# Kernel tuning notes

Hardware: AMD Instinct MI355X
Metric: run time of the kernel (lower is better)

## Reference

```python
import jax, jax.numpy as jnp
import numpy as np

B, N, D = 16, 1024, 768
NEG = -1.0e9

def leaky_relu(x, slope=0.01):
    return jnp.where(x >= 0, x, slope * x)

def setup_inputs() -> dict:
    key = jax.random.key(0)
    ks = jax.random.split(key, 20)
    s = 0.02
    inp = {
        'inputs': jax.random.normal(ks[0], (B, N, D), dtype=jnp.float32),
        'adj_mat': jax.random.randint(ks[1], (B, N, N), 0, 2).astype(jnp.float32),
        # BaseGraphAttNet params
        'W_fc': jax.random.normal(ks[2], (D, D), dtype=jnp.float32) * s,
        'b_fc': jnp.zeros((D,), dtype=jnp.float32),
        'w_q': jax.random.normal(ks[3], (D,), dtype=jnp.float32) * s,
        'b_q': jnp.zeros((), dtype=jnp.float32),
        'w_k': jax.random.normal(ks[4], (D,), dtype=jnp.float32) * s,
        'b_k': jnp.zeros((), dtype=jnp.float32),
        # gating params (6 linears)
        'W_uy': jax.random.normal(ks[5], (D, D), dtype=jnp.float32) * s,
        'b_uy': jnp.zeros((D,), dtype=jnp.float32),
        'W_ux': jax.random.normal(ks[6], (D, D), dtype=jnp.float32) * s,
        'b_ux': jnp.zeros((D,), dtype=jnp.float32),
        'W_ry': jax.random.normal(ks[7], (D, D), dtype=jnp.float32) * s,
        'b_ry': jnp.zeros((D,), dtype=jnp.float32),
        'W_rx': jax.random.normal(ks[8], (D, D), dtype=jnp.float32) * s,
        'b_rx': jnp.zeros((D,), dtype=jnp.float32),
        'W_ty': jax.random.normal(ks[9], (D, D), dtype=jnp.float32) * s,
        'b_ty': jnp.zeros((D,), dtype=jnp.float32),
        'W_tx': jax.random.normal(ks[10], (D, D), dtype=jnp.float32) * s,
        'b_tx': jnp.zeros((D,), dtype=jnp.float32),
    }
    return inp

def reference(inputs, adj_mat, W_fc, b_fc, w_q, b_q, w_k, b_k,
              W_uy, b_uy, W_ux, b_ux, W_ry, b_ry, W_rx, b_rx,
              W_ty, b_ty, W_tx, b_tx):
    # ---- BaseGraphAttNet (residual=False); dropout in eval mode (identity) ----
    feat_proj = jnp.einsum('bnd,ed->bne', inputs, W_fc) + b_fc      # bs x N x D
    q = jnp.einsum('bnd,d->bn', feat_proj, w_q) + b_q               # bs x N
    k = jnp.einsum('bnd,d->bn', feat_proj, w_k) + b_k               # bs x N
    logits = q[:, :, None] + k[:, None, :]                          # bs x N x N
    masked = logits + (1.0 - adj_mat) * NEG
    masked = leaky_relu(masked)
    att = jax.nn.softmax(masked, axis=-1)
    y = jnp.einsum('bnm,bmd->bnd', att, feat_proj)                  # bs x N x D
    # ---- GRU-style gating ----
    u = jax.nn.sigmoid(jnp.einsum('bnd,ed->bne', y, W_uy) + b_uy
                       + jnp.einsum('bnd,ed->bne', inputs, W_ux) + b_ux)
    r = jax.nn.sigmoid(jnp.einsum('bnd,ed->bne', y, W_ry) + b_ry
                       + jnp.einsum('bnd,ed->bne', inputs, W_rx) + b_rx)
    x_tmp = jnp.tanh(jnp.einsum('bnd,ed->bne', y, W_ty) + b_ty
                     + jnp.einsum('bnd,ed->bne', r * inputs, W_tx) + b_tx)
    out = (1.0 - u) * inputs + u * x_tmp
    return out
```

## Files before the change

### kernel.cpp

```cpp
#include <hip/hip_runtime.h>
#include <cmath>

typedef __attribute__((ext_vector_type(8))) short bf16x8;
typedef __attribute__((ext_vector_type(4))) float f32x4;
typedef unsigned short u16;

struct __align__(8) us4 { u16 x, y, z, w; };

__device__ __forceinline__ u16 f2bf(float f) {
    union { float f; unsigned u; } v; v.f = f;
    unsigned u = v.u;
    u += 0x7fffu + ((u >> 16) & 1u);
    return (u16)(u >> 16);
}
__device__ __forceinline__ float bf2f(u16 h) {
    union { unsigned u; float f; } v; v.u = ((unsigned)h) << 16;
    return v.f;
}
__device__ __forceinline__ float fast_tanh(float x) {
    float t = __expf(-2.f * fabsf(x));
    float th = (1.f - t) / (1.f + t);
    return copysignf(th, x);
}
__device__ __forceinline__ f32x4 mfma16(bf16x8 a, bf16x8 b, f32x4 c) {
    return __builtin_amdgcn_mfma_f32_16x16x32_bf16(a, b, c, 0, 0, 0);
}
__device__ __forceinline__ void ld_lds16(const u16* g, u16* l) {
    __builtin_amdgcn_global_load_lds(
        (const __attribute__((address_space(1))) unsigned int*)g,
        (__attribute__((address_space(3))) unsigned int*)l, 16, 0, 0);
}

__global__ __launch_bounds__(256) void cvtx(const float* __restrict__ in,
                                            u16* __restrict__ CatA, float* __restrict__ qkz) {
    int i = blockIdx.x * 256 + threadIdx.x;
    float4 f = reinterpret_cast<const float4*>(in)[i];
    us4 o; o.x = f2bf(f.x); o.y = f2bf(f.y); o.z = f2bf(f.z); o.w = f2bf(f.w);
    int row = i / 192, col = (i % 192) * 4;
    *reinterpret_cast<us4*>(CatA + (size_t)row * 1536 + 768 + col) = o;
    if (i < 8192) reinterpret_cast<float4*>(qkz)[i] = float4{0.f, 0.f, 0.f, 0.f};
}

struct WCvt { const float* s[7]; u16* d[7]; int ld[7]; };
__global__ __launch_bounds__(256) void cvtw(WCvt w) {
    int wi = blockIdx.y;
    int i = blockIdx.x * 256 + threadIdx.x;
    float4 f = reinterpret_cast<const float4*>(w.s[wi])[i];
    us4 o; o.x = f2bf(f.x); o.y = f2bf(f.y); o.z = f2bf(f.z); o.w = f2bf(f.w);
    int row = i / 192, col = (i % 192) * 4;
    *reinterpret_cast<us4*>(w.d[wi] + (size_t)row * w.ld[wi] + col) = o;
}

enum { EPI_FPT = 0, EPI_Y, EPI_GATES, EPI_OUT };

struct Epi {
    const float* b1; const float* b2; const float* b3; const float* b4;
    const float* wq; const float* wk; float* qv; float* kv;
    u16* fpT;
    u16* catA;
    const u16* xb;
    u16* ub_o; u16* rxb_o;
    const u16* ub; float* of;
};

template<int EPI, int PH>
__device__ __forceinline__ void g128_body(
    const u16* __restrict__ A1, const u16* __restrict__ B1,
    const u16* __restrict__ A2, const u16* __restrict__ B2,
    int K, int ldA1, int ldB1, int ldA2, int ldB2,
    size_t zA, size_t zB, Epi e)
{
    __shared__ u16 lA[128 * 64];
    __shared__ u16 lB[128 * 64];

    const int t = threadIdx.x;
    const int w = t >> 6, lane = t & 63, lm = lane & 15, quad = lane >> 4;
    const int row0 = blockIdx.x * 128;
    int col0, grp = 0;
    if constexpr (EPI == EPI_GATES) { grp = blockIdx.y / 6; col0 = (blockIdx.y % 6) * 128; }
    else col0 = blockIdx.y * 128;

    const int rs2 = t >> 3;
    const int kc2 = (((t & 7) ^ (rs2 & 7)) * 8);
    u16* dA_[4]; u16* dB_[4];
#pragma unroll
    for (int q = 0; q < 4; q++) {
        dA_[q] = lA + q * 2048 + w * 512;
        dB_[q] = lB + q * 2048 + w * 512;
    }

    const int rw0 = (w & 1) * 64, cw0 = (w >> 1) * 64;
    const int ch0 = ((quad) ^ (lm & 7)) * 8;
    const int ch1 = ((quad + 4) ^ (lm & 7)) * 8;
    int laB[4], lbB[4];
#pragma unroll
    for (int i = 0; i < 4; i++) laB[i] = (rw0 + i * 16 + lm) * 64;
#pragma unroll
    for (int j = 0; j < 4; j++) lbB[j] = (cw0 + j * 16 + lm) * 64;

    f32x4 acc[4][4] = {};
    bool first = true;

#pragma unroll
    for (int ph = 0; ph < PH; ph++) {
        const u16* As; const u16* Bs; int ldA, ldB;
        if (ph == 0) { As = A1 + (size_t)blockIdx.z * zA; Bs = B1 + (size_t)blockIdx.z * zB; ldA = ldA1; ldB = ldB1; }
        else         { As = A2; Bs = B2; ldA = ldA2; ldB = ldB2; }
        if constexpr (EPI == EPI_GATES) Bs += (size_t)grp * (768 * 1536);
        const u16* gA = As + (size_t)(row0 + rs2) * ldA + kc2;
        const u16* gB = Bs + (size_t)(col0 + rs2) * ldB + kc2;

        for (int k0 = 0; k0 < K; k0 += 64) {
            if (!first) __syncthreads();
            first = false;
#pragma unroll
            for (int q = 0; q < 4; q++) {
                ld_lds16(gA + (size_t)(q * 32) * ldA + k0, dA_[q]);
                ld_lds16(gB + (size_t)(q * 32) * ldB + k0, dB_[q]);
            }
            __syncthreads();

#pragma unroll
            for (int h = 0; h < 2; h++) {
                const int ch = h ? ch1 : ch0;
                bf16x8 a[4], b[4];
#pragma unroll
                for (int i = 0; i < 4; i++) a[i] = *reinterpret_cast<const bf16x8*>(lA + laB[i] + ch);
#pragma unroll
                for (int j = 0; j < 4; j++) b[j] = *reinterpret_cast<const bf16x8*>(lB + lbB[j] + ch);
#pragma unroll
                for (int i = 0; i < 4; i++)
#pragma unroll
                    for (int j = 0; j < 4; j++)
                        acc[i][j] = mfma16(a[i], b[j], acc[i][j]);
            }
        }
    }

#pragma unroll
    for (int i = 0; i < 4; i++) {
        const int gr = row0 + rw0 + i * 16 + quad * 4;
        if constexpr (EPI == EPI_FPT) {
            float qp[4] = {}, kp[4] = {};
            int bb = gr >> 10, nn = gr & 1023;
#pragma unroll
            for (int j = 0; j < 4; j++) {
                int gc = col0 + cw0 + j * 16 + lm;
                float bias = e.b1[gc];
                float v0 = acc[i][j][0] + bias, v1 = acc[i][j][1] + bias;
                float v2 = acc[i][j][2] + bias, v3 = acc[i][j][3] + bias;
                us4 o; o.x = f2bf(v0); o.y = f2bf(v1); o.z = f2bf(v2); o.w = f2bf(v3);
                *reinterpret_cast<us4*>(e.fpT + (size_t)bb * 786432 + (size_t)gc * 1024 + nn) = o;
                float wqv = e.wq[gc], wkv = e.wk[gc];
                qp[0] = fmaf(v0, wqv, qp[0]); qp[1] = fmaf(v1, wqv, qp[1]);
                qp[2] = fmaf(v2, wqv, qp[2]); qp[3] = fmaf(v3, wqv, qp[3]);
                kp[0] = fmaf(v0, wkv, kp[0]); kp[1] = fmaf(v1, wkv, kp[1]);
                kp[2] = fmaf(v2, wkv, kp[2]); kp[3] = fmaf(v3, wkv, kp[3]);
            }
#pragma unroll
            for (int r = 0; r < 4; r++) {
                float q = qp[r], k = kp[r];
#pragma unroll
                for (int m = 1; m < 16; m <<= 1) { q += __shfl_xor(q, m); k += __shfl_xor(k, m); }
                if (lm == 0) { atomicAdd(e.qv + gr + r, q); atomicAdd(e.kv + gr + r, k); }
            }
        } else if constexpr (EPI == EPI_Y) {
            size_t grow = (size_t)blockIdx.z * 1024 + gr;
#pragma unroll
            for (int j = 0; j < 4; j++) {
                int gc = col0 + cw0 + j * 16 + lm;
#pragma unroll
                for (int r = 0; r < 4; r++)
                    e.catA[(grow + r) * 1536 + gc] = f2bf(acc[i][j][r]);
            }
        } else if constexpr (EPI == EPI_GATES) {
#pragma unroll
            for (int j = 0; j < 4; j++) {
                int gc = col0 + cw0 + j * 16 + lm;
                if (grp == 0) {
                    float bias = e.b1[gc] + e.b2[gc];
#pragma unroll
                    for (int r = 0; r < 4; r++) {
                        size_t idx = (size_t)(gr + r) * 768 + gc;
                        e.ub_o[idx] = f2bf(1.f / (1.f + __expf(-(acc[i][j][r] + bias))));
                    }
                } else {
                    float bias = e.b3[gc] + e.b4[gc];
#pragma unroll
                    for (int r = 0; r < 4; r++) {
                        size_t idx = (size_t)(gr + r) * 768 + gc;
                        float rr = 1.f / (1.f + __expf(-(acc[i][j][r] + bias)));
                        float xv = bf2f(e.xb[(size_t)(gr + r) * 1536 + gc]);
                        e.rxb_o[idx] = f2bf(rr * xv);
                    }
                }
            }
        } else {
#pragma unroll
            for (int j = 0; j < 4; j++) {
                int gc = col0 + cw0 + j * 16 + lm;
                float bias = e.b1[gc] + e.b2[gc];
#pragma unroll
                for (int r = 0; r < 4; r++) {
                    size_t idx = (size_t)(gr + r) * 768 + gc;
                    float tt = fast_tanh(acc[i][j][r] + bias);
                    float uu = bf2f(e.ub[idx]);
                    float xv = bf2f(e.xb[(size_t)(gr + r) * 1536 + gc]);
                    __builtin_nontemporal_store((1.f - uu) * xv + uu * tt, e.of + idx);
                }
            }
        }
    }
}

__global__ __launch_bounds__(256) void gFPT(
    const u16* __restrict__ A1, const u16* __restrict__ B1, int K, int ldA1, int ldB1, Epi e) {
    g128_body<EPI_FPT, 1>(A1, B1, nullptr, nullptr, K, ldA1, ldB1, 0, 0, 0, 0, e);
}
__global__ __launch_bounds__(256) void gY(
    const u16* __restrict__ A1, const u16* __restrict__ B1, int K, int ldA1, int ldB1,
    size_t zA, size_t zB, Epi e) {
    g128_body<EPI_Y, 1>(A1, B1, nullptr, nullptr, K, ldA1, ldB1, 0, 0, zA, zB, e);
}
__global__ __launch_bounds__(256) void gGATES(
    const u16* __restrict__ A1, const u16* __restrict__ B1, int K, int ldA1, int ldB1, Epi e) {
    g128_body<EPI_GATES, 1>(A1, B1, nullptr, nullptr, K, ldA1, ldB1, 0, 0, 0, 0, e);
}
__global__ __launch_bounds__(256) void gOUT(
    const u16* __restrict__ A1, const u16* __restrict__ B1,
    const u16* __restrict__ A2, const u16* __restrict__ B2,
    int K, int ldA1, int ldB1, int ldA2, int ldB2, Epi e) {
    g128_body<EPI_OUT, 2>(A1, B1, A2, B2, K, ldA1, ldB1, ldA2, ldB2, 0, 0, e);
}

__global__ __launch_bounds__(256) void k_soft4(const float* __restrict__ adj,
                                               const float* __restrict__ qv,
                                               const float* __restrict__ kv,
                                               const float* __restrict__ bq,
                                               const float* __restrict__ bk,
                                               u16* __restrict__ attb) {
    int wv = threadIdx.x >> 6, lane = threadIdx.x & 63;
    int bn = blockIdx.x * 4 + wv;
    int b = bn >> 10;
    const float* adjrow = adj + (size_t)bn * 1024;
    const float* krow = kv + (b << 10);
    float q = qv[bn] + bq[0] + bk[0];

    float v[16];
#pragma unroll
    for (int c = 0; c < 4; c++) {
        float4 a4 = *reinterpret_cast<const float4*>(adjrow + c * 256 + lane * 4);
        float4 k4 = *reinterpret_cast<const float4*>(krow + c * 256 + lane * 4);
        float* vv = v + c * 4;
        vv[0] = q + k4.x + (1.f - a4.x) * -1.0e9f;
        vv[1] = q + k4.y + (1.f - a4.y) * -1.0e9f;
        vv[2] = q + k4.z + (1.f - a4.z) * -1.0e9f;
        vv[3] = q + k4.w + (1.f - a4.w) * -1.0e9f;
    }
#pragma unroll
    for (int t = 0; t < 16; t++) v[t] = v[t] >= 0.f ? v[t] : 0.01f * v[t];

    float mx = v[0];
#pragma unroll
    for (int t = 1; t < 16; t++) mx = fmaxf(mx, v[t]);
#pragma unroll
    for (int off = 32; off; off >>= 1) mx = fmaxf(mx, __shfl_xor(mx, off));

    float s = 0.f;
#pragma unroll
    for (int t = 0; t < 16; t++) { v[t] = __expf(v[t] - mx); s += v[t]; }
#pragma unroll
    for (int off = 32; off; off >>= 1) s += __shfl_xor(s, off);
    float inv = 1.f / s;

    u16* orow = attb + (size_t)bn * 1024;
#pragma unroll
    for (int c = 0; c < 4; c++) {
        us4 o;
        o.x = f2bf(v[c * 4 + 0] * inv); o.y = f2bf(v[c * 4 + 1] * inv);
        o.z = f2bf(v[c * 4 + 2] * inv); o.w = f2bf(v[c * 4 + 3] * inv);
        *reinterpret_cast<us4*>(orow + c * 256 + lane * 4) = o;
    }
}

extern "C" void kernel_launch(void* const* d_in, const int* in_sizes, int n_in,
                              void* d_out, int out_size, void* d_ws, size_t ws_size,
                              hipStream_t stream) {
    const float* x    = (const float*)d_in[0];
    const float* adj  = (const float*)d_in[1];
    const float* W_fc = (const float*)d_in[2];
    const float* b_fc = (const float*)d_in[3];
    const float* w_q  = (const float*)d_in[4];
    const float* b_q  = (const float*)d_in[5];
    const float* w_k  = (const float*)d_in[6];
    const float* b_k  = (const float*)d_in[7];
    const float* W_uy = (const float*)d_in[8];
    const float* b_uy = (const float*)d_in[9];
    const float* W_ux = (const float*)d_in[10];
    const float* b_ux = (const float*)d_in[11];
    const float* W_ry = (const float*)d_in[12];
    const float* b_ry = (const float*)d_in[13];
    const float* W_rx = (const float*)d_in[14];
    const float* b_rx = (const float*)d_in[15];
    const float* W_ty = (const float*)d_in[16];
    const float* b_ty = (const float*)d_in[17];
    const float* W_tx = (const float*)d_in[18];
    const float* b_tx = (const float*)d_in[19];

    char* ws = (char*)d_ws;
    u16*   CatA  = (u16*)  (ws + 0);
    u16*   Wfc_b = (u16*)  (ws + 50331648);
    u16*   Wty_b = (u16*)  (ws + 51511296);
    u16*   Wtx_b = (u16*)  (ws + 52690944);
    u16*   Wg    = (u16*)  (ws + 53870592);
    u16*   fpT   = (u16*)  (ws + 58589184);
    float* qv    = (float*)(ws + 83755008);
    float* kv    = (float*)(ws + 83820544);
    u16*   attb  = (u16*)  (ws + 83886080);
    u16*   u_b   = (u16*)  (ws + 83886080);
    u16*   rxb   = (u16*)  (ws + 117440512);

    cvtx<<<12288, 256, 0, stream>>>(x, CatA, qv);

    WCvt wc;
    wc.s[0] = W_fc; wc.d[0] = Wfc_b;              wc.ld[0] = 768;
    wc.s[1] = W_ty; wc.d[1] = Wty_b;              wc.ld[1] = 768;
    wc.s[2] = W_tx; wc.d[2] = Wtx_b;              wc.ld[2] = 768;
    wc.s[3] = W_uy; wc.d[3] = Wg;                 wc.ld[3] = 1536;
    wc.s[4] = W_ux; wc.d[4] = Wg + 768;           wc.ld[4] = 1536;
    wc.s[5] = W_ry; wc.d[5] = Wg + 768 * 1536;    wc.ld[5] = 1536;
    wc.s[6] = W_rx; wc.d[6] = Wg + 768 * 1536 + 768; wc.ld[6] = 1536;
    cvtw<<<dim3(576, 7), 256, 0, stream>>>(wc);

    Epi e{};
    e = Epi{}; e.b1 = b_fc; e.wq = w_q; e.wk = w_k; e.qv = qv; e.kv = kv; e.fpT = fpT;
    gFPT<<<dim3(128, 6), 256, 0, stream>>>(CatA + 768, Wfc_b, 768, 1536, 768, e);

    k_soft4<<<4096, 256, 0, stream>>>(adj, qv, kv, b_q, b_k, attb);

    e = Epi{}; e.catA = CatA;
    gY<<<dim3(8, 6, 16), 256, 0, stream>>>(attb, fpT, 1024, 1024, 1024,
                                           1048576, 786432, e);
    e = Epi{}; e.b1 = b_uy; e.b2 = b_ux; e.b3 = b_ry; e.b4 = b_rx;
    e.xb = CatA + 768; e.ub_o = u_b; e.rxb_o = rxb;
    gGATES<<<dim3(128, 12), 256, 0, stream>>>(CatA, Wg, 1536, 1536, 1536, e);

    e = Epi{}; e.b1 = b_ty; e.b2 = b_tx; e.ub = u_b; e.xb = CatA + 768; e.of = (float*)d_out;
    gOUT<<<dim3(128, 6), 256, 0, stream>>>(CatA, Wty_b, rxb, Wtx_b,
                                           768, 1536, 768, 768, 768, e);
}
```

Before: 419.1 us.

## Double-buffer LDS tiles in shared GEMM body to overlap loads with MFMA

The GEMM body now uses two LDS buffers per operand and issues the global-to-LDS loads for the next K-tile before computing on the current one. This replaces the old load, sync, compute, sync loop with a single barrier per tile. The two-phase path (gOUT) becomes one flat tile index over both operand pairs. Shared memory per block doubles to 64 KB, which may lower occupancy.

```diff
diff --git a/kernel.cpp b/kernel.cpp
--- a/kernel.cpp
+++ b/kernel.cpp
@@ -63,15 +63,15 @@
     const u16* ub; float* of;
 };
 
-template<int EPI, int PH>
+template<int EPI>
 __device__ __forceinline__ void g128_body(
     const u16* __restrict__ A1, const u16* __restrict__ B1,
     const u16* __restrict__ A2, const u16* __restrict__ B2,
-    int K, int ldA1, int ldB1, int ldA2, int ldB2,
+    int nt1, int nt2, int ldA1, int ldB1, int ldA2, int ldB2,
     size_t zA, size_t zB, Epi e)
 {
-    __shared__ u16 lA[128 * 64];
-    __shared__ u16 lB[128 * 64];
+    __shared__ u16 lA[2 * 8192];
+    __shared__ u16 lB[2 * 8192];
 
     const int t = threadIdx.x;
     const int w = t >> 6, lane = t & 63, lm = lane & 15, quad = lane >> 4;
@@ -80,14 +80,28 @@
     if constexpr (EPI == EPI_GATES) { grp = blockIdx.y / 6; col0 = (blockIdx.y % 6) * 128; }
     else col0 = blockIdx.y * 128;
 
+    const u16* A1p = A1 + (size_t)blockIdx.z * zA;
+    const u16* B1p = B1 + (size_t)blockIdx.z * zB;
+    if constexpr (EPI == EPI_GATES) B1p += (size_t)grp * (768 * 1536);
+    const int NT = nt1 + nt2;
+
     const int rs2 = t >> 3;
     const int kc2 = (((t & 7) ^ (rs2 & 7)) * 8);
-    u16* dA_[4]; u16* dB_[4];
-#pragma unroll
-    for (int q = 0; q < 4; q++) {
-        dA_[q] = lA + q * 2048 + w * 512;
-        dB_[q] = lB + q * 2048 + w * 512;
-    }
+
+    auto stage = [&](int ti, int bi) {
+        const u16 *Sa, *Sb; int la_, lb_, k0;
+        if (ti < nt1) { Sa = A1p; Sb = B1p; la_ = ldA1; lb_ = ldB1; k0 = ti * 64; }
+        else          { Sa = A2;  Sb = B2;  la_ = ldA2; lb_ = ldB2; k0 = (ti - nt1) * 64; }
+        const u16* gA = Sa + (size_t)(row0 + rs2) * la_ + k0 + kc2;
+        const u16* gB = Sb + (size_t)(col0 + rs2) * lb_ + k0 + kc2;
+        u16* dA = lA + bi * 8192 + w * 512;
+        u16* dB = lB + bi * 8192 + w * 512;
+#pragma unroll
+        for (int q = 0; q < 4; q++) {
+            ld_lds16(gA + (size_t)(q * 32) * la_, dA + q * 2048);
+            ld_lds16(gB + (size_t)(q * 32) * lb_, dB + q * 2048);
+        }
+    };
 
     const int rw0 = (w & 1) * 64, cw0 = (w >> 1) * 64;
     const int ch0 = ((quad) ^ (lm & 7)) * 8;
@@ -99,42 +113,31 @@
     for (int j = 0; j < 4; j++) lbB[j] = (cw0 + j * 16 + lm) * 64;
 
     f32x4 acc[4][4] = {};
-    bool first = true;
-
-#pragma unroll
-    for (int ph = 0; ph < PH; ph++) {
-        const u16* As; const u16* Bs; int ldA, ldB;
-        if (ph == 0) { As = A1 + (size_t)blockIdx.z * zA; Bs = B1 + (size_t)blockIdx.z * zB; ldA = ldA1; ldB = ldB1; }
-        else         { As = A2; Bs = B2; ldA = ldA2; ldB = ldB2; }
-        if constexpr (EPI == EPI_GATES) Bs += (size_t)grp * (768 * 1536);
-        const u16* gA = As + (size_t)(row0 + rs2) * ldA + kc2;
-        const u16* gB = Bs + (size_t)(col0 + rs2) * ldB + kc2;
-
-        for (int k0 = 0; k0 < K; k0 += 64) {
-            if (!first) __syncthreads();
-            first = false;
-#pragma unroll
-            for (int q = 0; q < 4; q++) {
-                ld_lds16(gA + (size_t)(q * 32) * ldA + k0, dA_[q]);
-                ld_lds16(gB + (size_t)(q * 32) * ldB + k0, dB_[q]);
-            }
-            __syncthreads();
-
-#pragma unroll
-            for (int h = 0; h < 2; h++) {
-                const int ch = h ? ch1 : ch0;
-                bf16x8 a[4], b[4];
-#pragma unroll
-                for (int i = 0; i < 4; i++) a[i] = *reinterpret_cast<const bf16x8*>(lA + laB[i] + ch);
-#pragma unroll
-                for (int j = 0; j < 4; j++) b[j] = *reinterpret_cast<const bf16x8*>(lB + lbB[j] + ch);
-#pragma unroll
-                for (int i = 0; i < 4; i++)
-#pragma unroll
-                    for (int j = 0; j < 4; j++)
-                        acc[i][j] = mfma16(a[i], b[j], acc[i][j]);
-            }
+
+    stage(0, 0);
+    __syncthreads();
+
+    int cur = 0;
+    for (int ti = 0; ti < NT; ++ti) {
+        if (ti + 1 < NT) stage(ti + 1, cur ^ 1);
+        const u16* bA = lA + cur * 8192;
+        const u16* bB = lB + cur * 8192;
+#pragma unroll
+        for (int h = 0; h < 2; h++) {
+            const int ch = h ? ch1 : ch0;
+            bf16x8 a[4], b[4];
+#pragma unroll
+            for (int i = 0; i < 4; i++) a[i] = *reinterpret_cast<const bf16x8*>(bA + laB[i] + ch);
+#pragma unroll
+            for (int j = 0; j < 4; j++) b[j] = *reinterpret_cast<const bf16x8*>(bB + lbB[j] + ch);
+#pragma unroll
+            for (int i = 0; i < 4; i++)
+#pragma unroll
+                for (int j = 0; j < 4; j++)
+                    acc[i][j] = mfma16(a[i], b[j], acc[i][j]);
         }
+        __syncthreads();
+        cur ^= 1;
     }
 
 #pragma unroll
@@ -214,23 +217,23 @@
 }
 
 __global__ __launch_bounds__(256) void gFPT(
-    const u16* __restrict__ A1, const u16* __restrict__ B1, int K, int ldA1, int ldB1, Epi e) {
-    g128_body<EPI_FPT, 1>(A1, B1, nullptr, nullptr, K, ldA1, ldB1, 0, 0, 0, 0, e);
+    const u16* __restrict__ A1, const u16* __restrict__ B1, int nt1, int ldA1, int ldB1, Epi e) {
+    g128_body<EPI_FPT>(A1, B1, nullptr, nullptr, nt1, 0, ldA1, ldB1, 0, 0, 0, 0, e);
 }
 __global__ __launch_bounds__(256) void gY(
-    const u16* __restrict__ A1, const u16* __restrict__ B1, int K, int ldA1, int ldB1,
+    const u16* __restrict__ A1, const u16* __restrict__ B1, int nt1, int ldA1, int ldB1,
     size_t zA, size_t zB, Epi e) {
-    g128_body<EPI_Y, 1>(A1, B1, nullptr, nullptr, K, ldA1, ldB1, 0, 0, zA, zB, e);
+    g128_body<EPI_Y>(A1, B1, nullptr, nullptr, nt1, 0, ldA1, ldB1, 0, 0, zA, zB, e);
 }
 __global__ __launch_bounds__(256) void gGATES(
-    const u16* __restrict__ A1, const u16* __restrict__ B1, int K, int ldA1, int ldB1, Epi e) {
-    g128_body<EPI_GATES, 1>(A1, B1, nullptr, nullptr, K, ldA1, ldB1, 0, 0, 0, 0, e);
+    const u16* __restrict__ A1, const u16* __restrict__ B1, int nt1, int ldA1, int ldB1, Epi e) {
+    g128_body<EPI_GATES>(A1, B1, nullptr, nullptr, nt1, 0, ldA1, ldB1, 0, 0, 0, 0, e);
 }
 __global__ __launch_bounds__(256) void gOUT(
     const u16* __restrict__ A1, const u16* __restrict__ B1,
     const u16* __restrict__ A2, const u16* __restrict__ B2,
-    int K, int ldA1, int ldB1, int ldA2, int ldB2, Epi e) {
-    g128_body<EPI_OUT, 2>(A1, B1, A2, B2, K, ldA1, ldB1, ldA2, ldB2, 0, 0, e);
+    int nt1, int nt2, int ldA1, int ldB1, int ldA2, int ldB2, Epi e) {
+    g128_body<EPI_OUT>(A1, B1, A2, B2, nt1, nt2, ldA1, ldB1, ldA2, ldB2, 0, 0, e);
 }
 
 __global__ __launch_bounds__(256) void k_soft4(const float* __restrict__ adj,
@@ -334,18 +337,19 @@
 
     Epi e{};
     e = Epi{}; e.b1 = b_fc; e.wq = w_q; e.wk = w_k; e.qv = qv; e.kv = kv; e.fpT = fpT;
-    gFPT<<<dim3(128, 6), 256, 0, stream>>>(CatA + 768, Wfc_b, 768, 1536, 768, e);
+    gFPT<<<dim3(128, 6), 256, 0, stream>>>(CatA + 768, Wfc_b, 12, 1536, 768, e);
 
     k_soft4<<<4096, 256, 0, stream>>>(adj, qv, kv, b_q, b_k, attb);
 
     e = Epi{}; e.catA = CatA;
-    gY<<<dim3(8, 6, 16), 256, 0, stream>>>(attb, fpT, 1024, 1024, 1024,
+    gY<<<dim3(8, 6, 16), 256, 0, stream>>>(attb, fpT, 16, 1024, 1024,
                                            1048576, 786432, e);
+
     e = Epi{}; e.b1 = b_uy; e.b2 = b_ux; e.b3 = b_ry; e.b4 = b_rx;
     e.xb = CatA + 768; e.ub_o = u_b; e.rxb_o = rxb;
-    gGATES<<<dim3(128, 12), 256, 0, stream>>>(CatA, Wg, 1536, 1536, 1536, e);
+    gGATES<<<dim3(128, 12), 256, 0, stream>>>(CatA, Wg, 24, 1536, 1536, e);
 
     e = Epi{}; e.b1 = b_ty; e.b2 = b_tx; e.ub = u_b; e.xb = CatA + 768; e.of = (float*)d_out;
     gOUT<<<dim3(128, 6), 256, 0, stream>>>(CatA, Wty_b, rxb, Wtx_b,
-                                           768, 1536, 768, 768, 768, e);
-}
+                                           12, 12, 1536, 768, 768, 768, e);
+}
```

New measurement: 466.4 us. 11.3% more time.
